# Kernel optimization log

Measured on AMD Instinct MI355X. Metric: run time of the kernel, lower is better.

## Reference

```python
import jax, jax.numpy as jnp
import numpy as np

D_MODEL = 1024
N_HEADS = 16
HEAD_DIM = D_MODEL // N_HEADS


def rotate_half(x):
    # interleaved rotate: (-x_odd, x_even) re-interleaved
    x1 = x[..., ::2]
    x2 = x[..., 1::2]
    return jnp.stack((-x2, x1), axis=-1).reshape(x.shape)


def rope_tables(seq_len, dim, dtype):
    inv_freq = 1.0 / (10000.0 ** (jnp.arange(0, dim, 2, dtype=jnp.float32) / dim))
    t = jnp.arange(seq_len, dtype=jnp.float32)
    freqs = jnp.einsum('i,j->ij', t, inv_freq)          # [T, dim/2]
    emb = jnp.concatenate((freqs, freqs), axis=-1)       # [T, dim]
    return jnp.cos(emb).astype(dtype)[None, None], jnp.sin(emb).astype(dtype)[None, None]


def setup_inputs() -> dict:
    key = jax.random.key(0)
    k1, k2, k3 = jax.random.split(key, 3)
    B, T, C = 2, 2048, D_MODEL
    scale_in = 1.0 / np.sqrt(C)
    return {
        'x': jax.random.normal(k1, (B, T, C), dtype=jnp.float32),
        'attention_mask': jnp.ones((B, T), dtype=jnp.int32),
        'qkv_w': jax.random.normal(k2, (3 * C, C), dtype=jnp.float32) * scale_in,
        'qkv_b': jnp.zeros((3 * C,), dtype=jnp.float32),
        'out_w': jax.random.normal(k3, (C, C), dtype=jnp.float32) * scale_in,
        'out_b': jnp.zeros((C,), dtype=jnp.float32),
    }


def reference(x, attention_mask, qkv_w, qkv_b, out_w, out_b):
    B, T, C = x.shape
    H, Dh = N_HEADS, HEAD_DIM
    qkv = x @ qkv_w.T + qkv_b                             # [B,T,3C]
    q, k, v = jnp.split(qkv, 3, axis=-1)
    q = q.reshape(B, T, H, Dh).transpose(0, 2, 1, 3)      # [B,H,T,Dh]
    k = k.reshape(B, T, H, Dh).transpose(0, 2, 1, 3)
    v = v.reshape(B, T, H, Dh).transpose(0, 2, 1, 3)
    cos, sin = rope_tables(T, Dh, x.dtype)                # [1,1,T,Dh]
    q = q * cos + rotate_half(q) * sin
    k = k * cos + rotate_half(k) * sin
    att = jnp.einsum('bhqd,bhkd->bhqk', q, k) / jnp.sqrt(jnp.array(Dh, x.dtype))
    causal = jnp.tril(jnp.ones((T, T), dtype=bool))[None, None]
    key_mask = attention_mask.astype(bool)[:, None, None, :]
    neg_inf = jnp.array(-jnp.inf, att.dtype)
    att = jnp.where(causal & key_mask, att, neg_inf)
    att = jax.nn.softmax(att, axis=-1)
    query_mask = attention_mask.astype(bool)[:, None, :, None]
    att = att * query_mask
    y = jnp.einsum('bhqk,bhkd->bhqd', att, v)             # [B,H,T,Dh]
    y = y.transpose(0, 2, 1, 3).reshape(B, T, C)
    y = y * attention_mask[:, :, None].astype(y.dtype)
    y = y @ out_w.T + out_b
    return y
```

## Files before the change

kernel.cpp:

```cpp
#include <hip/hip_runtime.h>
#include <hip/hip_bf16.h>

typedef __bf16 bf16;
typedef __bf16 bf16x4 __attribute__((ext_vector_type(4)));
typedef __bf16 bf16x8 __attribute__((ext_vector_type(8)));
typedef float f32x4 __attribute__((ext_vector_type(4)));
typedef unsigned int u32x4 __attribute__((ext_vector_type(4)));

#define T_LEN 2048
#define NHEAD 16
#define DHEAD 64
#define CDIM 1024
#define NB 2

__device__ __forceinline__ void g2l16(const void* g, void* l) {
    __builtin_amdgcn_global_load_lds(
        (const __attribute__((address_space(1))) unsigned int*)g,
        (__attribute__((address_space(3))) unsigned int*)l, 16, 0, 0);
}

__device__ __forceinline__ float fexp2(float x) {
    float r;
    asm("v_exp_f32 %0, %1" : "=v"(r) : "v"(x));
    return r;
}

__device__ __forceinline__ void stage_swz256(const bf16* __restrict__ g, size_t gstride,
                                             bf16* lds, int t) {
#pragma unroll
    for (int c = 0; c < 2; c++) {
        int off = c * 4096 + t * 16;
        int row = off >> 7;
        int lcol = (off & 127) ^ ((row & 7) << 4);
        g2l16(g + (size_t)row * gstride + (lcol >> 1), (char*)lds + off);
    }
}

__device__ __forceinline__ bf16x8 rd_swz(const bf16* lds, int row, int colB) {
    return *(const bf16x8*)((const char*)lds + row * 128 + (colB ^ ((row & 7) << 4)));
}

__global__ __launch_bounds__(256) void prep_kernel(
    const float* __restrict__ x, const float* __restrict__ qkv_w,
    const float* __restrict__ out_w, const int* __restrict__ am,
    bf16* __restrict__ xb, bf16* __restrict__ wqb, bf16* __restrict__ wob,
    float* __restrict__ ct, float* __restrict__ st, float* __restrict__ mf,
    int* __restrict__ mflag) {
    int bid = blockIdx.x;
    if (bid < 4096) {
        int i = bid * 256 + threadIdx.x;
        const float* src; bf16* dst; int j;
        if (i < 524288)      { src = x;     dst = xb;  j = i; }
        else if (i < 917504) { src = qkv_w; dst = wqb; j = i - 524288; }
        else                 { src = out_w; dst = wob; j = i - 917504; }
        const float4* p = (const float4*)src + (size_t)j * 2;
        float4 a = p[0], b = p[1];
        bf16x8 o;
        o[0] = (bf16)a.x; o[1] = (bf16)a.y; o[2] = (bf16)a.z; o[3] = (bf16)a.w;
        o[4] = (bf16)b.x; o[5] = (bf16)b.y; o[6] = (bf16)b.z; o[7] = (bf16)b.w;
        ((bf16x8*)dst)[j] = o;
    } else if (bid < 4608) {
        int i = (bid - 4096) * 256 + threadIdx.x;
        int t = i >> 6, d = i & 63;
        float ex = (float)(2 * (d & 31)) / 64.0f;
        float inv = powf(10000.0f, -ex);
        float ang = (float)t * inv;
        ct[i] = cosf(ang);
        st[i] = sinf(ang);
    } else {
        int i = (bid - 4608) * 256 + threadIdx.x;
        int v = am[i];
        mf[i] = (v != 0) ? 0.0f : -1e30f;
        unsigned long long bz = __ballot(v == 0);
        if ((threadIdx.x & 63) == 0) mflag[i >> 6] = (bz != 0) ? 1 : 0;
    }
}

__global__ __launch_bounds__(512, 4) void gemm_qkv_kernel(
    const bf16* __restrict__ xb, const bf16* __restrict__ wb,
    const float* __restrict__ bias,
    const float* __restrict__ ct, const float* __restrict__ st,
    bf16* __restrict__ qg, bf16* __restrict__ kg, bf16* __restrict__ vt) {
    __shared__ __align__(16) bf16 smem[2][2 * 128 * 64];
    int m0 = blockIdx.x * 128, n0 = blockIdx.y * 128;
    int t = threadIdx.x, w = t >> 6, l = t & 63;
    int wm = w & 3, wn = w >> 2;
    int l15 = l & 15, lhi = l >> 4;
    f32x4 acc[2][4] = {};
#pragma unroll
    for (int c = 0; c < 2; c++) {
        int off = c * 8192 + t * 16;
        int row = off >> 7;
        int lcol = (off & 127) ^ ((row & 7) << 4);
        g2l16(xb + (size_t)(m0 + row) * CDIM + (lcol >> 1), (char*)smem[0] + off);
        g2l16(wb + (size_t)(n0 + row) * CDIM + (lcol >> 1), (char*)(smem[0] + 128 * 64) + off);
    }
    __syncthreads();
    int cur = 0;
    for (int k0 = 0; k0 < CDIM; k0 += 64) {
        if (k0 + 64 < CDIM) {
#pragma unroll
            for (int c = 0; c < 2; c++) {
                int off = c * 8192 + t * 16;
                int row = off >> 7;
                int lcol = (off & 127) ^ ((row & 7) << 4);
                g2l16(xb + (size_t)(m0 + row) * CDIM + k0 + 64 + (lcol >> 1),
                      (char*)smem[cur ^ 1] + off);
                g2l16(wb + (size_t)(n0 + row) * CDIM + k0 + 64 + (lcol >> 1),
                      (char*)(smem[cur ^ 1] + 128 * 64) + off);
            }
        }
        bf16* sA = smem[cur];
        bf16* sB = smem[cur] + 128 * 64;
#pragma unroll
        for (int ks = 0; ks < 2; ks++) {
            bf16x8 af[2], bfr[4];
#pragma unroll
            for (int mt = 0; mt < 2; mt++)
                af[mt] = rd_swz(sA, wm * 32 + mt * 16 + l15, ks * 64 + lhi * 16);
#pragma unroll
            for (int nt = 0; nt < 4; nt++)
                bfr[nt] = rd_swz(sB, wn * 64 + nt * 16 + l15, ks * 64 + lhi * 16);
#pragma unroll
            for (int mt = 0; mt < 2; mt++)
#pragma unroll
                for (int nt = 0; nt < 4; nt++)
                    acc[mt][nt] = __builtin_amdgcn_mfma_f32_16x16x32_bf16(
                        af[mt], bfr[nt], acc[mt][nt], 0, 0, 0);
        }
        __syncthreads();
        cur ^= 1;
    }
    int bb = m0 >> 11, tt0 = m0 & 2047;
    if (n0 >= 2048) {
        bf16* sT = (bf16*)smem;
#pragma unroll
        for (int pass = 0; pass < 2; pass++) {
            __syncthreads();
            if (wn == pass) {
#pragma unroll
                for (int nt = 0; nt < 4; nt++) {
                    int dl = nt * 16 + l15;
                    float cb = bias[n0 + pass * 64 + dl];
#pragma unroll
                    for (int mt = 0; mt < 2; mt++) {
                        bf16x4 pv;
#pragma unroll
                        for (int r = 0; r < 4; r++) pv[r] = (bf16)(acc[mt][nt][r] + cb);
                        *(bf16x4*)(sT + dl * 136 + wm * 32 + mt * 16 + lhi * 4) = pv;
                    }
                }
            }
            __syncthreads();
            int h_p = ((n0 & 1023) >> 6) + pass;
            size_t vbase = ((size_t)(bb * NHEAD + h_p)) * T_LEN * DHEAD + tt0;
#pragma unroll
            for (int c = 0; c < 2; c++) {
                int cid = c * 512 + t;
                int d = cid >> 4, ch = cid & 15;
                *(bf16x8*)(vt + vbase + (size_t)d * T_LEN + ch * 8) =
                    *(const bf16x8*)(sT + d * 136 + ch * 8);
            }
        }
        return;
    }
    int sec = n0 >> 10;
    bf16* og = (sec == 0) ? qg : kg;
    float oscale = (sec == 0) ? 0.125f * 1.44269504f : 1.0f;
#pragma unroll
    for (int nt = 0; nt < 4; nt++) {
        int col = n0 + wn * 64 + nt * 16 + l15;
        int cc = col & 1023;
        int h = cc >> 6, d = cc & 63;
        float cb = bias[col];
        size_t hb = ((size_t)(bb * NHEAD + h)) * T_LEN * DHEAD;
#pragma unroll
        for (int mt = 0; mt < 2; mt++) {
#pragma unroll
            for (int r = 0; r < 4; r++) {
                int tt = tt0 + wm * 32 + mt * 16 + lhi * 4 + r;
                float v = acc[mt][nt][r] + cb;
                float p = __shfl_xor(v, 1);
                float cs = ct[tt * 64 + d], sn = st[tt * 64 + d];
                float o = (d & 1) ? (v * cs + p * sn) : (v * cs - p * sn);
                og[hb + (size_t)tt * DHEAD + d] = (bf16)(o * oscale);
            }
        }
    }
}

__global__ __launch_bounds__(256, 4) void attn_kernel(
    const bf16* __restrict__ qg, const bf16* __restrict__ kg, const bf16* __restrict__ vt,
    const float* __restrict__ maskf, const int* __restrict__ mflag,
    bf16* __restrict__ yb) {
    __shared__ __align__(16) bf16 sK[2][64 * 64];
    __shared__ __align__(16) bf16 sV[2][64 * 64];
    int lin = blockIdx.x;
    int xcd = lin & 7, idx = lin >> 3;
    int group = idx >> 4, pos = idx & 15;
    int pair = xcd * 4 + group;
    int h = pair & 15, b = pair >> 4;
    int t = threadIdx.x, w = t >> 6, l = t & 63;
    int l15 = l & 15, lhi = l >> 4;
    const size_t head_off = ((size_t)(b * NHEAD + h)) * T_LEN * DHEAD;
    const bf16* qb = qg + head_off;
    const bf16* kb = kg + head_off;
    const bf16* vb = vt + head_off;
    const float* mrow = maskf + b * T_LEN;
    const int* mfl = mflag + b * (T_LEN / 64);
    const u32x4 onesu = {0x3F803F80u, 0x3F803F80u, 0x3F803F80u, 0x3F803F80u};
    const bf16x8 ones8 = __builtin_bit_cast(bf16x8, onesu);
#pragma unroll 1
    for (int ph = 0; ph < 2; ph++) {
        int qt = ph ? (31 - pos) : pos;
        int q0 = qt * 64;
        const int wq0 = q0 + w * 16;
        const int qrow_l = wq0 + l15;
        bf16x8 qf[2];
        qf[0] = *(const bf16x8*)(qb + (size_t)qrow_l * DHEAD + lhi * 8);
        qf[1] = *(const bf16x8*)(qb + (size_t)qrow_l * DHEAD + 32 + lhi * 8);
        f32x4 lsv = {};
        f32x4 accy[4] = {};
        stage_swz256(kb, DHEAD, sK[0], t);
        stage_swz256(vb, T_LEN, sV[0], t);
        __syncthreads();
        int cur = 0;
        for (int kv0 = 0; kv0 <= q0; kv0 += 64) {
            if (kv0 + 64 <= q0) {
                stage_swz256(kb + (size_t)(kv0 + 64) * DHEAD, DHEAD, sK[cur ^ 1], t);
                stage_swz256(vb + (kv0 + 64), T_LEN, sV[cur ^ 1], t);
            }
            if (kv0 <= wq0 + 15) {
                f32x4 s[4] = {};
                __builtin_amdgcn_s_setprio(1);
#pragma unroll
                for (int c = 0; c < 4; c++)
#pragma unroll
                    for (int ks = 0; ks < 2; ks++) {
                        bf16x8 kf = rd_swz(sK[cur], c * 16 + l15, ks * 64 + lhi * 16);
                        s[c] = __builtin_amdgcn_mfma_f32_16x16x32_bf16(kf, qf[ks], s[c], 0, 0, 0);
                    }
                __builtin_amdgcn_s_setprio(0);
                bool diag = (kv0 + 63 > wq0);
                int needmask = mfl[kv0 >> 6];
                if (needmask || diag) {
#pragma unroll
                    for (int c = 0; c < 4; c++) {
                        float mpv[4] = {0.f, 0.f, 0.f, 0.f};
                        if (needmask) {
                            float4 mq = *(const float4*)(mrow + kv0 + c * 16 + lhi * 4);
                            mpv[0] = mq.x; mpv[1] = mq.y; mpv[2] = mq.z; mpv[3] = mq.w;
                        }
#pragma unroll
                        for (int r = 0; r < 4; r++) {
                            float sv = s[c][r] + mpv[r];
                            if (diag && (kv0 + c * 16 + lhi * 4 + r > qrow_l)) sv = -1e30f;
                            s[c][r] = sv;
                        }
                    }
                }
#pragma unroll
                for (int c = 0; c < 4; c++)
#pragma unroll
                    for (int r = 0; r < 4; r++) s[c][r] = fexp2(s[c][r]);
                __builtin_amdgcn_s_setprio(1);
#pragma unroll
                for (int g2 = 0; g2 < 2; g2++) {
                    unsigned a0, a1, b0, b1;
                    asm("v_cvt_pk_bf16_f32 %0, %1, %2" : "=v"(a0) : "v"(s[2 * g2][0]), "v"(s[2 * g2][1]));
                    asm("v_cvt_pk_bf16_f32 %0, %1, %2" : "=v"(a1) : "v"(s[2 * g2][2]), "v"(s[2 * g2][3]));
                    asm("v_cvt_pk_bf16_f32 %0, %1, %2" : "=v"(b0) : "v"(s[2 * g2 + 1][0]), "v"(s[2 * g2 + 1][1]));
                    asm("v_cvt_pk_bf16_f32 %0, %1, %2" : "=v"(b1) : "v"(s[2 * g2 + 1][2]), "v"(s[2 * g2 + 1][3]));
                    asm("v_permlane32_swap_b32 %0, %1" : "+v"(a0), "+v"(b0));
                    asm("v_permlane16_swap_b32 %0, %1" : "+v"(a0), "+v"(b0));
                    asm("v_permlane32_swap_b32 %0, %1" : "+v"(a1), "+v"(b1));
                    asm("v_permlane16_swap_b32 %0, %1" : "+v"(a1), "+v"(b1));
                    u32x4 pu;
                    pu[0] = a0; pu[1] = a1; pu[2] = b0; pu[3] = b1;
                    bf16x8 pv = __builtin_bit_cast(bf16x8, pu);
                    lsv = __builtin_amdgcn_mfma_f32_16x16x32_bf16(pv, ones8, lsv, 0, 0, 0);
#pragma unroll
                    for (int dt = 0; dt < 4; dt++) {
                        bf16x8 vf = rd_swz(sV[cur], dt * 16 + l15, g2 * 64 + lhi * 16);
                        accy[dt] = __builtin_amdgcn_mfma_f32_16x16x32_bf16(pv, vf, accy[dt], 0, 0, 0);
                    }
                }
                __builtin_amdgcn_s_setprio(0);
            }
            __syncthreads();
            cur ^= 1;
        }
#pragma unroll
        for (int r = 0; r < 4; r++) {
            float inv = lsv[r] > 0.f ? 1.0f / lsv[r] : 0.0f;
            int rowt = wq0 + lhi * 4 + r;
            size_t obase = ((size_t)(b * T_LEN + rowt)) * CDIM + (size_t)h * DHEAD;
#pragma unroll
            for (int dt = 0; dt < 4; dt++)
                yb[obase + dt * 16 + l15] = (bf16)(accy[dt][r] * inv);
        }
        __syncthreads();
    }
}

__global__ __launch_bounds__(256) void gemm_out_kernel(
    const bf16* __restrict__ yb, const bf16* __restrict__ wb,
    const float* __restrict__ bias, float* __restrict__ out) {
    __shared__ __align__(16) bf16 smem[2][128 * 64 + 64 * 64];
    int m0 = blockIdx.x * 128, n0 = blockIdx.y * 64;
    int t = threadIdx.x, w = t >> 6, l = t & 63;
    int wm = w >> 1, wn = w & 1;
    int l15 = l & 15, lhi = l >> 4;
    f32x4 acc[4][2] = {};
#pragma unroll
    for (int i = 0; i < 4; i++) {
        int off = i * 4096 + t * 16;
        int row = off >> 7;
        int lcol = (off & 127) ^ ((row & 7) << 4);
        g2l16(yb + (size_t)(m0 + row) * CDIM + (lcol >> 1), (char*)smem[0] + off);
        if (i < 2)
            g2l16(wb + (size_t)(n0 + row) * CDIM + (lcol >> 1),
                  (char*)(smem[0] + 128 * 64) + off);
    }
    __syncthreads();
    int cur = 0;
    for (int k0 = 0; k0 < CDIM; k0 += 64) {
        if (k0 + 64 < CDIM) {
#pragma unroll
            for (int i = 0; i < 4; i++) {
                int off = i * 4096 + t * 16;
                int row = off >> 7;
                int lcol = (off & 127) ^ ((row & 7) << 4);
                g2l16(yb + (size_t)(m0 + row) * CDIM + k0 + 64 + (lcol >> 1),
                      (char*)smem[cur ^ 1] + off);
                if (i < 2)
                    g2l16(wb + (size_t)(n0 + row) * CDIM + k0 + 64 + (lcol >> 1),
                          (char*)(smem[cur ^ 1] + 128 * 64) + off);
            }
        }
        bf16* sA = smem[cur];
        bf16* sB = smem[cur] + 128 * 64;
#pragma unroll
        for (int ks = 0; ks < 2; ks++) {
            bf16x8 af[4], bfr[2];
#pragma unroll
            for (int mt = 0; mt < 4; mt++)
                af[mt] = rd_swz(sA, wm * 64 + mt * 16 + l15, ks * 64 + lhi * 16);
#pragma unroll
            for (int nt = 0; nt < 2; nt++)
                bfr[nt] = rd_swz(sB, wn * 32 + nt * 16 + l15, ks * 64 + lhi * 16);
#pragma unroll
            for (int mt = 0; mt < 4; mt++)
#pragma unroll
                for (int nt = 0; nt < 2; nt++)
                    acc[mt][nt] = __builtin_amdgcn_mfma_f32_16x16x32_bf16(
                        af[mt], bfr[nt], acc[mt][nt], 0, 0, 0);
        }
        __syncthreads();
        cur ^= 1;
    }
#pragma unroll
    for (int nt = 0; nt < 2; nt++) {
        int col = n0 + wn * 32 + nt * 16 + l15;
        float cb = bias[col];
#pragma unroll
        for (int mt = 0; mt < 4; mt++) {
#pragma unroll
            for (int r = 0; r < 4; r++) {
                int rowm = m0 + wm * 64 + mt * 16 + lhi * 4 + r;
                out[(size_t)rowm * CDIM + col] = acc[mt][nt][r] + cb;
            }
        }
    }
}

extern "C" void kernel_launch(void* const* d_in, const int* in_sizes, int n_in,
                              void* d_out, int out_size, void* d_ws, size_t ws_size,
                              hipStream_t stream) {
    const float* x      = (const float*)d_in[0];
    const int*   amask  = (const int*)d_in[1];
    const float* qkv_w  = (const float*)d_in[2];
    const float* qkv_b  = (const float*)d_in[3];
    const float* out_w  = (const float*)d_in[4];
    const float* out_b  = (const float*)d_in[5];
    float* out = (float*)d_out;

    char* ws = (char*)d_ws;
    bf16* xb  = (bf16*)(ws);
    bf16* wqb = (bf16*)(ws + (8ull  << 20));
    bf16* wob = (bf16*)(ws + (14ull << 20));
    bf16* qg  = (bf16*)(ws + (16ull << 20));
    bf16* kg  = (bf16*)(ws + (24ull << 20));
    bf16* vt  = (bf16*)(ws + (32ull << 20));
    bf16* yb  = (bf16*)(ws + (40ull << 20));
    float* ctab = (float*)(ws + (48ull << 20));
    float* stab = (float*)(ws + (48ull << 20) + (1ull << 19));
    float* mkf  = (float*)(ws + (49ull << 20));
    int*   mfg  = (int*)(ws + (49ull << 20) + (16ull << 10));

    prep_kernel<<<4624, 256, 0, stream>>>(x, qkv_w, out_w, amask,
                                          xb, wqb, wob, ctab, stab, mkf, mfg);
    gemm_qkv_kernel<<<dim3(32, 24), 512, 0, stream>>>(xb, wqb, qkv_b, ctab, stab, qg, kg, vt);
    attn_kernel<<<dim3(512), 256, 0, stream>>>(qg, kg, vt, mkf, mfg, yb);
    gemm_out_kernel<<<dim3(32, 16), 256, 0, stream>>>(yb, wob, out_b, out);
}
```

Baseline: 97.18 us.

## Process one 128-row query tile per block with two 16-row MFMA blocks per wave

Replaces the two-phase scheme, where each block handled two balanced 64-row query tiles in sequence, with a single 128-row query tile per block. Each wave now owns 32 query rows as two 16-row sub-blocks that share every K and V fragment read from shared memory. This halves K/V staging and LDS reads per query row and removes the phase restart overhead. In exchange it uses more registers per wave, and per-block work becomes uneven across the causal triangle. The imbalance is only partly offset by reversing tile order for alternate groups.

```diff
diff --git a/kernel.cpp b/kernel.cpp
--- a/kernel.cpp
+++ b/kernel.cpp
@@ -198,8 +198,10 @@
     int lin = blockIdx.x;
     int xcd = lin & 7, idx = lin >> 3;
     int group = idx >> 4, pos = idx & 15;
+    int qt = (group & 2) ? (15 - pos) : pos;
     int pair = xcd * 4 + group;
     int h = pair & 15, b = pair >> 4;
+    int q0 = qt * 128;
     int t = threadIdx.x, w = t >> 6, l = t & 63;
     int l15 = l & 15, lhi = l >> 4;
     const size_t head_off = ((size_t)(b * NHEAD + h)) * T_LEN * DHEAD;
@@ -208,42 +210,50 @@
     const bf16* vb = vt + head_off;
     const float* mrow = maskf + b * T_LEN;
     const int* mfl = mflag + b * (T_LEN / 64);
+    const int wq0 = q0 + w * 32;
+    bf16x8 qf[2][2];
+#pragma unroll
+    for (int mb = 0; mb < 2; mb++) {
+        int qr = wq0 + mb * 16 + l15;
+        qf[mb][0] = *(const bf16x8*)(qb + (size_t)qr * DHEAD + lhi * 8);
+        qf[mb][1] = *(const bf16x8*)(qb + (size_t)qr * DHEAD + 32 + lhi * 8);
+    }
     const u32x4 onesu = {0x3F803F80u, 0x3F803F80u, 0x3F803F80u, 0x3F803F80u};
     const bf16x8 ones8 = __builtin_bit_cast(bf16x8, onesu);
-#pragma unroll 1
-    for (int ph = 0; ph < 2; ph++) {
-        int qt = ph ? (31 - pos) : pos;
-        int q0 = qt * 64;
-        const int wq0 = q0 + w * 16;
-        const int qrow_l = wq0 + l15;
-        bf16x8 qf[2];
-        qf[0] = *(const bf16x8*)(qb + (size_t)qrow_l * DHEAD + lhi * 8);
-        qf[1] = *(const bf16x8*)(qb + (size_t)qrow_l * DHEAD + 32 + lhi * 8);
-        f32x4 lsv = {};
-        f32x4 accy[4] = {};
-        stage_swz256(kb, DHEAD, sK[0], t);
-        stage_swz256(vb, T_LEN, sV[0], t);
-        __syncthreads();
-        int cur = 0;
-        for (int kv0 = 0; kv0 <= q0; kv0 += 64) {
-            if (kv0 + 64 <= q0) {
-                stage_swz256(kb + (size_t)(kv0 + 64) * DHEAD, DHEAD, sK[cur ^ 1], t);
-                stage_swz256(vb + (kv0 + 64), T_LEN, sV[cur ^ 1], t);
-            }
-            if (kv0 <= wq0 + 15) {
-                f32x4 s[4] = {};
-                __builtin_amdgcn_s_setprio(1);
-#pragma unroll
-                for (int c = 0; c < 4; c++)
-#pragma unroll
-                    for (int ks = 0; ks < 2; ks++) {
-                        bf16x8 kf = rd_swz(sK[cur], c * 16 + l15, ks * 64 + lhi * 16);
-                        s[c] = __builtin_amdgcn_mfma_f32_16x16x32_bf16(kf, qf[ks], s[c], 0, 0, 0);
-                    }
-                __builtin_amdgcn_s_setprio(0);
-                bool diag = (kv0 + 63 > wq0);
-                int needmask = mfl[kv0 >> 6];
+    f32x4 lsv[2] = {};
+    f32x4 accy[2][4] = {};
+    stage_swz256(kb, DHEAD, sK[0], t);
+    stage_swz256(vb, T_LEN, sV[0], t);
+    __syncthreads();
+    int cur = 0;
+    const int kv_end = q0 + 64;
+    for (int kv0 = 0; kv0 <= kv_end; kv0 += 64) {
+        if (kv0 + 64 <= kv_end) {
+            stage_swz256(kb + (size_t)(kv0 + 64) * DHEAD, DHEAD, sK[cur ^ 1], t);
+            stage_swz256(vb + (kv0 + 64), T_LEN, sV[cur ^ 1], t);
+        }
+        if (kv0 <= wq0 + 31) {
+            const bool act0 = (kv0 <= wq0 + 15);
+            f32x4 s[2][4] = {};
+            __builtin_amdgcn_s_setprio(1);
+#pragma unroll
+            for (int c = 0; c < 4; c++)
+#pragma unroll
+                for (int ks = 0; ks < 2; ks++) {
+                    bf16x8 kf = rd_swz(sK[cur], c * 16 + l15, ks * 64 + lhi * 16);
+                    if (act0)
+                        s[0][c] = __builtin_amdgcn_mfma_f32_16x16x32_bf16(kf, qf[0][ks], s[0][c], 0, 0, 0);
+                    s[1][c] = __builtin_amdgcn_mfma_f32_16x16x32_bf16(kf, qf[1][ks], s[1][c], 0, 0, 0);
+                }
+            __builtin_amdgcn_s_setprio(0);
+            int needmask = mfl[kv0 >> 6];
+#pragma unroll
+            for (int mb = 0; mb < 2; mb++) {
+                if (mb == 0 && !act0) continue;
+                int mq0 = wq0 + mb * 16;
+                bool diag = (kv0 + 63 > mq0);
                 if (needmask || diag) {
+                    int qrow_l = mq0 + l15;
 #pragma unroll
                     for (int c = 0; c < 4; c++) {
                         float mpv[4] = {0.f, 0.f, 0.f, 0.f};
@@ -253,54 +263,62 @@
                         }
 #pragma unroll
                         for (int r = 0; r < 4; r++) {
-                            float sv = s[c][r] + mpv[r];
+                            float sv = s[mb][c][r] + mpv[r];
                             if (diag && (kv0 + c * 16 + lhi * 4 + r > qrow_l)) sv = -1e30f;
-                            s[c][r] = sv;
+                            s[mb][c][r] = sv;
                         }
                     }
                 }
 #pragma unroll
                 for (int c = 0; c < 4; c++)
 #pragma unroll
-                    for (int r = 0; r < 4; r++) s[c][r] = fexp2(s[c][r]);
-                __builtin_amdgcn_s_setprio(1);
-#pragma unroll
-                for (int g2 = 0; g2 < 2; g2++) {
+                    for (int r = 0; r < 4; r++) s[mb][c][r] = fexp2(s[mb][c][r]);
+            }
+            __builtin_amdgcn_s_setprio(1);
+#pragma unroll
+            for (int g2 = 0; g2 < 2; g2++) {
+                bf16x8 pvm[2];
+#pragma unroll
+                for (int mb = 0; mb < 2; mb++) {
+                    if (mb == 0 && !act0) continue;
                     unsigned a0, a1, b0, b1;
-                    asm("v_cvt_pk_bf16_f32 %0, %1, %2" : "=v"(a0) : "v"(s[2 * g2][0]), "v"(s[2 * g2][1]));
-                    asm("v_cvt_pk_bf16_f32 %0, %1, %2" : "=v"(a1) : "v"(s[2 * g2][2]), "v"(s[2 * g2][3]));
-                    asm("v_cvt_pk_bf16_f32 %0, %1, %2" : "=v"(b0) : "v"(s[2 * g2 + 1][0]), "v"(s[2 * g2 + 1][1]));
-                    asm("v_cvt_pk_bf16_f32 %0, %1, %2" : "=v"(b1) : "v"(s[2 * g2 + 1][2]), "v"(s[2 * g2 + 1][3]));
+                    asm("v_cvt_pk_bf16_f32 %0, %1, %2" : "=v"(a0) : "v"(s[mb][2 * g2][0]), "v"(s[mb][2 * g2][1]));
+                    asm("v_cvt_pk_bf16_f32 %0, %1, %2" : "=v"(a1) : "v"(s[mb][2 * g2][2]), "v"(s[mb][2 * g2][3]));
+                    asm("v_cvt_pk_bf16_f32 %0, %1, %2" : "=v"(b0) : "v"(s[mb][2 * g2 + 1][0]), "v"(s[mb][2 * g2 + 1][1]));
+                    asm("v_cvt_pk_bf16_f32 %0, %1, %2" : "=v"(b1) : "v"(s[mb][2 * g2 + 1][2]), "v"(s[mb][2 * g2 + 1][3]));
                     asm("v_permlane32_swap_b32 %0, %1" : "+v"(a0), "+v"(b0));
                     asm("v_permlane16_swap_b32 %0, %1" : "+v"(a0), "+v"(b0));
                     asm("v_permlane32_swap_b32 %0, %1" : "+v"(a1), "+v"(b1));
                     asm("v_permlane16_swap_b32 %0, %1" : "+v"(a1), "+v"(b1));
                     u32x4 pu;
                     pu[0] = a0; pu[1] = a1; pu[2] = b0; pu[3] = b1;
-                    bf16x8 pv = __builtin_bit_cast(bf16x8, pu);
-                    lsv = __builtin_amdgcn_mfma_f32_16x16x32_bf16(pv, ones8, lsv, 0, 0, 0);
-#pragma unroll
-                    for (int dt = 0; dt < 4; dt++) {
-                        bf16x8 vf = rd_swz(sV[cur], dt * 16 + l15, g2 * 64 + lhi * 16);
-                        accy[dt] = __builtin_amdgcn_mfma_f32_16x16x32_bf16(pv, vf, accy[dt], 0, 0, 0);
-                    }
+                    pvm[mb] = __builtin_bit_cast(bf16x8, pu);
+                    lsv[mb] = __builtin_amdgcn_mfma_f32_16x16x32_bf16(pvm[mb], ones8, lsv[mb], 0, 0, 0);
                 }
-                __builtin_amdgcn_s_setprio(0);
-            }
-            __syncthreads();
-            cur ^= 1;
-        }
+#pragma unroll
+                for (int dt = 0; dt < 4; dt++) {
+                    bf16x8 vf = rd_swz(sV[cur], dt * 16 + l15, g2 * 64 + lhi * 16);
+                    if (act0)
+                        accy[0][dt] = __builtin_amdgcn_mfma_f32_16x16x32_bf16(pvm[0], vf, accy[0][dt], 0, 0, 0);
+                    accy[1][dt] = __builtin_amdgcn_mfma_f32_16x16x32_bf16(pvm[1], vf, accy[1][dt], 0, 0, 0);
+                }
+            }
+            __builtin_amdgcn_s_setprio(0);
+        }
+        __syncthreads();
+        cur ^= 1;
+    }
+#pragma unroll
+    for (int mb = 0; mb < 2; mb++)
 #pragma unroll
         for (int r = 0; r < 4; r++) {
-            float inv = lsv[r] > 0.f ? 1.0f / lsv[r] : 0.0f;
-            int rowt = wq0 + lhi * 4 + r;
+            float inv = lsv[mb][r] > 0.f ? 1.0f / lsv[mb][r] : 0.0f;
+            int rowt = wq0 + mb * 16 + lhi * 4 + r;
             size_t obase = ((size_t)(b * T_LEN + rowt)) * CDIM + (size_t)h * DHEAD;
 #pragma unroll
             for (int dt = 0; dt < 4; dt++)
-                yb[obase + dt * 16 + l15] = (bf16)(accy[dt][r] * inv);
-        }
-        __syncthreads();
-    }
+                yb[obase + dt * 16 + l15] = (bf16)(accy[mb][dt][r] * inv);
+        }
 }
 
 __global__ __launch_bounds__(256) void gemm_out_kernel(
```

Result: slower. 118.0 us (+21.5%).
